# Kernel tuning notes

Measured on AMD Instinct MI355X. Metric: run time of the kernel, lower is better.

Reference implementation:

```python
import jax, jax.numpy as jnp
import numpy as np

NUM_ROUTING = 3
EPS = 1e-8

def squash(s, axis=-1):
    # v = (||s||^2 / (1 + ||s||^2)) * s / ||s||
    n2 = jnp.sum(jnp.square(s), axis=axis, keepdims=True)
    scale = n2 / (1.0 + n2) / jnp.sqrt(n2 + EPS)
    return scale * s

def setup_inputs() -> dict:
    key = jax.random.key(0)
    k1, k2 = jax.random.split(key)
    B, IN_CAPS, IN_DIM = 64, 2048, 16
    NUM_CAPS, DIM = 16, 16
    inputs = jax.random.normal(k1, (B, IN_CAPS, IN_DIM), dtype=jnp.float32)
    # xavier_uniform over last two dims (fan_in=IN_DIM, fan_out=DIM)
    limit = float(np.sqrt(6.0 / (IN_DIM + DIM)))
    W = jax.random.uniform(k2, (IN_CAPS, NUM_CAPS, IN_DIM, DIM), dtype=jnp.float32,
                           minval=-limit, maxval=limit)
    return {"inputs": inputs, "W": W}

def reference(inputs, W):
    # inputs: [B, I, N] ; W: [I, J, N, M] ; inputs_hat: [B, I, J, M]
    inputs_hat = jnp.einsum('ijnm,bin->bijm', W, inputs)
    B, I, J, M = inputs_hat.shape
    b = jnp.zeros((B, I, J), dtype=inputs_hat.dtype)
    outputs = None
    for i in range(NUM_ROUTING):
        c = jax.nn.softmax(b, axis=-1)               # coupling coeffs over output capsules j
        s = jnp.einsum('bij,bijm->bjm', c, inputs_hat)
        outputs = squash(s)                          # [B, J, M]
        if i < NUM_ROUTING - 1:
            b = b + jnp.einsum('bjm,bijm->bij', outputs, inputs_hat)
    return outputs
```

## Files before the change

### kernel.cpp

```cpp
#include <hip/hip_runtime.h>
#include <math.h>

#define BATCH 64
#define IC 2048
#define NI 16
#define NB 16
#define NG (IC / NI)
#define NBG (BATCH / NB)

template <bool FIRST>
__global__ __launch_bounds__(256, 2) void pass_kernel(
    const float* __restrict__ Wt,
    const float* __restrict__ inp,
    const float* __restrict__ vcum,
    float* __restrict__ partial)
{
    const int tid = threadIdx.x;
    const int j = tid & 15;
    const int m = tid >> 4;
    const int g = blockIdx.x & (NG - 1);
    const int bg = blockIdx.x >> 7;
    const int i0 = g * NI;
    const int b0 = bg * NB;
    const int wave = tid >> 6;
    const int lane = tid & 63;

    __shared__ float w_lds[16 * 260];
    __shared__ float red[2][4][16];
    __shared__ float outx[2][17 * 16];

    float vc[NB];
    if (!FIRST) {
#pragma unroll
        for (int b = 0; b < NB; ++b)
            vc[b] = vcum[(b0 + b) * 256 + j * 16 + m];
    }

    float acc[NB];
#pragma unroll
    for (int b = 0; b < NB; ++b) acc[b] = 0.0f;

    for (int ii = 0; ii < NI; ++ii) {
        const int i = i0 + ii;
        const float4* wg = (const float4*)(Wt + (size_t)i * 4096 + (size_t)tid * 16);
        float4 a0 = wg[0], a1 = wg[1], a2 = wg[2], a3 = wg[3];
        __syncthreads();
        {
            float* dst = &w_lds[(tid >> 4) * 260 + (tid & 15) * 16];
            *(float4*)(dst + 0) = a0;
            *(float4*)(dst + 4) = a1;
            *(float4*)(dst + 8) = a2;
            *(float4*)(dst + 12) = a3;
        }
        __syncthreads();
        float w[16];
#pragma unroll
        for (int n = 0; n < 16; ++n)
            w[n] = w_lds[j * 260 + n * 16 + m];

#pragma unroll
        for (int b = 0; b < NB; ++b) {
            const float4* up = (const float4*)(inp + ((size_t)(b0 + b) * IC + i) * 16);
            float4 ua = up[0], ub = up[1], uc = up[2], ud = up[3];
            float p0 = w[0] * ua.x;  p0 = fmaf(w[1], ua.y, p0);
            p0 = fmaf(w[2], ua.z, p0);  p0 = fmaf(w[3], ua.w, p0);
            float p1 = w[4] * ub.x;  p1 = fmaf(w[5], ub.y, p1);
            p1 = fmaf(w[6], ub.z, p1);  p1 = fmaf(w[7], ub.w, p1);
            float p2 = w[8] * uc.x;  p2 = fmaf(w[9], uc.y, p2);
            p2 = fmaf(w[10], uc.z, p2); p2 = fmaf(w[11], uc.w, p2);
            float p3 = w[12] * ud.x; p3 = fmaf(w[13], ud.y, p3);
            p3 = fmaf(w[14], ud.z, p3); p3 = fmaf(w[15], ud.w, p3);
            const float hat = (p0 + p1) + (p2 + p3);

            if (FIRST) {
                acc[b] += hat;
            } else {
                float t = vc[b] * hat;
                t += __shfl_xor(t, 16);
                t += __shfl_xor(t, 32);
                if (lane < 16) red[b & 1][wave][lane] = t;
                __syncthreads();
                const float logit = red[b & 1][0][j] + red[b & 1][1][j] +
                                    red[b & 1][2][j] + red[b & 1][3][j];
                const float e = __expf(logit);
                float s = e;
                s += __shfl_xor(s, 1);
                s += __shfl_xor(s, 2);
                s += __shfl_xor(s, 4);
                s += __shfl_xor(s, 8);
                const float c = e * __builtin_amdgcn_rcpf(s);
                acc[b] = fmaf(c, hat, acc[b]);
            }
        }
    }

#pragma unroll
    for (int b = 0; b < NB; ++b) {
        if (b < 2) __syncthreads();
        outx[b & 1][j * 17 + m] = acc[b];
        __syncthreads();
        partial[((size_t)g * BATCH + (b0 + b)) * 256 + tid] =
            outx[b & 1][(tid >> 4) * 17 + (tid & 15)];
    }
}

__global__ __launch_bounds__(256) void reduce_squash(
    const float* __restrict__ partial, float* __restrict__ vcum,
    float* __restrict__ out, int stage)
{
    const int b = blockIdx.x;
    const int tid = threadIdx.x;
    const float* p = partial + (size_t)b * 256 + tid;
    float s = 0.0f;
#pragma unroll 4
    for (int gi = 0; gi < NG; ++gi)
        s += p[(size_t)gi * BATCH * 256];
    if (stage == 0) s *= (1.0f / 16.0f);

    float n2 = s * s;
    n2 += __shfl_xor(n2, 1);
    n2 += __shfl_xor(n2, 2);
    n2 += __shfl_xor(n2, 4);
    n2 += __shfl_xor(n2, 8);
    const float scale = n2 / ((1.0f + n2) * sqrtf(n2 + 1e-8f));
    const float v = scale * s;

    const int o = b * 256 + tid;
    if (stage == 0)      vcum[o] = v;
    else if (stage == 1) vcum[o] += v;
    else                 out[o] = v;
}

extern "C" void kernel_launch(void* const* d_in, const int* in_sizes, int n_in,
                              void* d_out, int out_size, void* d_ws, size_t ws_size,
                              hipStream_t stream) {
    const float* inp = (const float*)d_in[0];
    const float* Wt  = (const float*)d_in[1];
    float* out = (float*)d_out;
    float* partial = (float*)d_ws;
    float* vcum = partial + (size_t)NG * BATCH * 256;

    const dim3 gp(NG * NBG), bp(256);

    pass_kernel<true><<<gp, bp, 0, stream>>>(Wt, inp, nullptr, partial);
    reduce_squash<<<BATCH, 256, 0, stream>>>(partial, vcum, out, 0);
    pass_kernel<false><<<gp, bp, 0, stream>>>(Wt, inp, vcum, partial);
    reduce_squash<<<BATCH, 256, 0, stream>>>(partial, vcum, out, 1);
    pass_kernel<false><<<gp, bp, 0, stream>>>(Wt, inp, vcum, partial);
    reduce_squash<<<BATCH, 256, 0, stream>>>(partial, vcum, out, 2);
}
```

Baseline: 478.1 us.

## Remap pass kernel so each wave owns batches and lanes compute four m outputs

Each wave now handles two batch elements, with each lane computing four m outputs as float4 for one output capsule j. This keeps the routing-logit dot product inside a single wave, so the per-batch __syncthreads and LDS reduction go away. Weights are loaded straight from global memory as float4 instead of being staged through LDS, and partial results are written directly as float4 without the LDS transpose. The batch tile per block drops from 16 to 8, doubling the grid and raising the launch-bounds occupancy hint to 4. In exchange, W is re-read from global/L2 by every wave and every block, and register pressure goes up.

```diff
diff --git a/kernel.cpp b/kernel.cpp
--- a/kernel.cpp
+++ b/kernel.cpp
@@ -4,104 +4,87 @@
 #define BATCH 64
 #define IC 2048
 #define NI 16
-#define NB 16
 #define NG (IC / NI)
-#define NBG (BATCH / NB)
+#define NBPB 8
+#define NBG (BATCH / NBPB)
 
 template <bool FIRST>
-__global__ __launch_bounds__(256, 2) void pass_kernel(
+__global__ __launch_bounds__(256, 4) void pass_kernel(
     const float* __restrict__ Wt,
     const float* __restrict__ inp,
     const float* __restrict__ vcum,
     float* __restrict__ partial)
 {
-    const int tid = threadIdx.x;
-    const int j = tid & 15;
-    const int m = tid >> 4;
-    const int g = blockIdx.x & (NG - 1);
-    const int bg = blockIdx.x >> 7;
-    const int i0 = g * NI;
-    const int b0 = bg * NB;
+    const int tid  = threadIdx.x;
     const int wave = tid >> 6;
     const int lane = tid & 63;
+    const int j    = lane & 15;
+    const int mg   = lane >> 4;
+    const int g    = blockIdx.x & (NG - 1);
+    const int bg   = blockIdx.x >> 7;
+    const int i0   = g * NI;
+    const int bbase = bg * NBPB + wave * 2;
 
-    __shared__ float w_lds[16 * 260];
-    __shared__ float red[2][4][16];
-    __shared__ float outx[2][17 * 16];
-
-    float vc[NB];
+    float4 vc[2];
     if (!FIRST) {
 #pragma unroll
-        for (int b = 0; b < NB; ++b)
-            vc[b] = vcum[(b0 + b) * 256 + j * 16 + m];
+        for (int bb = 0; bb < 2; ++bb)
+            vc[bb] = *(const float4*)(vcum + (bbase + bb) * 256 + j * 16 + mg * 4);
     }
 
-    float acc[NB];
-#pragma unroll
-    for (int b = 0; b < NB; ++b) acc[b] = 0.0f;
+    float4 acc[2];
+    acc[0] = make_float4(0.f, 0.f, 0.f, 0.f);
+    acc[1] = make_float4(0.f, 0.f, 0.f, 0.f);
 
     for (int ii = 0; ii < NI; ++ii) {
         const int i = i0 + ii;
-        const float4* wg = (const float4*)(Wt + (size_t)i * 4096 + (size_t)tid * 16);
-        float4 a0 = wg[0], a1 = wg[1], a2 = wg[2], a3 = wg[3];
-        __syncthreads();
-        {
-            float* dst = &w_lds[(tid >> 4) * 260 + (tid & 15) * 16];
-            *(float4*)(dst + 0) = a0;
-            *(float4*)(dst + 4) = a1;
-            *(float4*)(dst + 8) = a2;
-            *(float4*)(dst + 12) = a3;
-        }
-        __syncthreads();
-        float w[16];
+        const float4* wp = (const float4*)(Wt + (size_t)i * 4096 + j * 256 + mg * 4);
+        float4 w[16];
 #pragma unroll
-        for (int n = 0; n < 16; ++n)
-            w[n] = w_lds[j * 260 + n * 16 + m];
+        for (int n = 0; n < 16; ++n) w[n] = wp[n * 4];
 
 #pragma unroll
-        for (int b = 0; b < NB; ++b) {
-            const float4* up = (const float4*)(inp + ((size_t)(b0 + b) * IC + i) * 16);
-            float4 ua = up[0], ub = up[1], uc = up[2], ud = up[3];
-            float p0 = w[0] * ua.x;  p0 = fmaf(w[1], ua.y, p0);
-            p0 = fmaf(w[2], ua.z, p0);  p0 = fmaf(w[3], ua.w, p0);
-            float p1 = w[4] * ub.x;  p1 = fmaf(w[5], ub.y, p1);
-            p1 = fmaf(w[6], ub.z, p1);  p1 = fmaf(w[7], ub.w, p1);
-            float p2 = w[8] * uc.x;  p2 = fmaf(w[9], uc.y, p2);
-            p2 = fmaf(w[10], uc.z, p2); p2 = fmaf(w[11], uc.w, p2);
-            float p3 = w[12] * ud.x; p3 = fmaf(w[13], ud.y, p3);
-            p3 = fmaf(w[14], ud.z, p3); p3 = fmaf(w[15], ud.w, p3);
-            const float hat = (p0 + p1) + (p2 + p3);
+        for (int bb = 0; bb < 2; ++bb) {
+            const int b = bbase + bb;
+            const float4* up = (const float4*)(inp + ((size_t)b * IC + i) * 16);
+            float4 u0 = up[0], u1 = up[1], u2 = up[2], u3 = up[3];
+
+            float4 h = make_float4(0.f, 0.f, 0.f, 0.f);
+#define ACC4(W, S)                                                     \
+            h.x = fmaf((W).x, (S), h.x); h.y = fmaf((W).y, (S), h.y);  \
+            h.z = fmaf((W).z, (S), h.z); h.w = fmaf((W).w, (S), h.w);
+            ACC4(w[0],  u0.x) ACC4(w[1],  u0.y) ACC4(w[2],  u0.z) ACC4(w[3],  u0.w)
+            ACC4(w[4],  u1.x) ACC4(w[5],  u1.y) ACC4(w[6],  u1.z) ACC4(w[7],  u1.w)
+            ACC4(w[8],  u2.x) ACC4(w[9],  u2.y) ACC4(w[10], u2.z) ACC4(w[11], u2.w)
+            ACC4(w[12], u3.x) ACC4(w[13], u3.y) ACC4(w[14], u3.z) ACC4(w[15], u3.w)
+#undef ACC4
 
             if (FIRST) {
-                acc[b] += hat;
+                acc[bb].x += h.x; acc[bb].y += h.y;
+                acc[bb].z += h.z; acc[bb].w += h.w;
             } else {
-                float t = vc[b] * hat;
+                float t = h.x * vc[bb].x + h.y * vc[bb].y +
+                          h.z * vc[bb].z + h.w * vc[bb].w;
                 t += __shfl_xor(t, 16);
                 t += __shfl_xor(t, 32);
-                if (lane < 16) red[b & 1][wave][lane] = t;
-                __syncthreads();
-                const float logit = red[b & 1][0][j] + red[b & 1][1][j] +
-                                    red[b & 1][2][j] + red[b & 1][3][j];
-                const float e = __expf(logit);
+                const float e = __expf(t);
                 float s = e;
                 s += __shfl_xor(s, 1);
                 s += __shfl_xor(s, 2);
                 s += __shfl_xor(s, 4);
                 s += __shfl_xor(s, 8);
                 const float c = e * __builtin_amdgcn_rcpf(s);
-                acc[b] = fmaf(c, hat, acc[b]);
+                acc[bb].x = fmaf(c, h.x, acc[bb].x);
+                acc[bb].y = fmaf(c, h.y, acc[bb].y);
+                acc[bb].z = fmaf(c, h.z, acc[bb].z);
+                acc[bb].w = fmaf(c, h.w, acc[bb].w);
             }
         }
     }
 
 #pragma unroll
-    for (int b = 0; b < NB; ++b) {
-        if (b < 2) __syncthreads();
-        outx[b & 1][j * 17 + m] = acc[b];
-        __syncthreads();
-        partial[((size_t)g * BATCH + (b0 + b)) * 256 + tid] =
-            outx[b & 1][(tid >> 4) * 17 + (tid & 15)];
-    }
+    for (int bb = 0; bb < 2; ++bb)
+        *(float4*)(partial + ((size_t)g * BATCH + (bbase + bb)) * 256 + j * 16 + mg * 4) = acc[bb];
 }
 
 __global__ __launch_bounds__(256) void reduce_squash(
```

Result: no change. 487.6 us (+2.0%).
